# Performance work log

Measured on AMD Instinct MI355X. Metric: run time of the kernel, lower is better.

## Reference

```python
import jax, jax.numpy as jnp
import numpy as np


def setup_inputs() -> dict:
    key = jax.random.key(0)
    ks = jax.random.split(key, 6)
    B, C, H, W = 4, 64, 96, 96
    IC = C // 2
    return {
        "x": jax.random.normal(ks[0], (B, C, H, W), dtype=jnp.float32),
        "y": jax.random.normal(ks[1], (B, C, H, W), dtype=jnp.float32),
        "w_phi": jax.random.normal(ks[2], (IC, C), dtype=jnp.float32) * 0.05,
        "w_theta": jax.random.normal(ks[3], (IC, C), dtype=jnp.float32) * 0.05,
        "w_g": jax.random.normal(ks[4], (IC, C), dtype=jnp.float32) * 0.05,
        "w_mask": jax.random.normal(ks[5], (C, IC), dtype=jnp.float32) * 0.05,
    }


def reference(x, y, w_phi, w_theta, w_g, w_mask):
    # x, y: [B, C, H, W]; 1x1 convs (no bias) are channel GEMMs.
    B, C, H, W = x.shape
    IC = C // 2
    # conv outputs have IC channels, but the original views them as (B, C, -1),
    # i.e. token axis N = IC*H*W / C = H*W/2, feature axis C. Replicate exactly.
    phi = jnp.einsum('bchw,oc->bohw', x, w_phi).reshape(B, C, -1)          # [B, C, N]
    theta = jnp.einsum('bchw,oc->bohw', y, w_theta).reshape(B, C, -1)      # [B, C, N]
    theta = jnp.transpose(theta, (0, 2, 1))                                # [B, N, C]
    g = jnp.einsum('bchw,oc->bohw', x, w_g).reshape(B, C, -1)              # [B, C, N]
    g = jnp.transpose(g, (0, 2, 1))                                        # [B, N, C]
    scores = jnp.einsum('bnc,bcm->bnm', theta, phi)                        # [B, N, N]
    attn = jax.nn.softmax(scores, axis=1)  # softmax over dim=1 (rows), per original
    out = jnp.einsum('bnm,bmc->bnc', attn, g)                              # [B, N, C]
    out = jnp.transpose(out, (0, 2, 1)).reshape(B, IC, H, W)               # [B, IC, H, W]
    mask = jnp.einsum('bchw,oc->bohw', out, w_mask)                        # [B, C, H, W]
    return mask + x
```

## Files before the change

kernel.cpp:

```cpp
#include <hip/hip_runtime.h>

#define NTOK 4608
#define CCH  64
#define HWSZ 9216
#define NB   4
#define NSPL 8
#define NCHT (NTOK/32)
#define L2E  1.4426950408889634f

typedef unsigned short u16;
typedef __attribute__((ext_vector_type(4))) short s16x4;
typedef __attribute__((ext_vector_type(8))) short s16x8;
typedef __attribute__((ext_vector_type(4))) float f32x4;

__device__ __forceinline__ f32x4 mfma16(s16x8 a, s16x8 b, f32x4 c){
  return __builtin_amdgcn_mfma_f32_16x16x32_bf16(a, b, c, 0, 0, 0);
}
__device__ __forceinline__ short f2bfh(float f){
  __bf16 h = (__bf16)f;
  return (short)__builtin_bit_cast(unsigned short, h);
}
__device__ __forceinline__ float bf2f(u16 h){
  return __uint_as_float(((unsigned int)h) << 16);
}
__device__ __forceinline__ float ex2(float x){
  return __builtin_amdgcn_exp2f(x);
}

__device__ __forceinline__ void gload16(const void* g, void* l){
  __builtin_amdgcn_global_load_lds(
      (const __attribute__((address_space(1))) void*)g,
      (__attribute__((address_space(3))) void*)l, 16, 0, 0);
}
#define SBAR() __builtin_amdgcn_sched_barrier(0)
#define WAITVM(N) do{ SBAR(); asm volatile("s_waitcnt vmcnt(" #N ")" ::: "memory"); SBAR(); }while(0)
#define PRIO(N) __builtin_amdgcn_s_setprio(N)

__global__ __launch_bounds__(512) void proj_kernel(
    const float* __restrict__ x, const float* __restrict__ y,
    const float* __restrict__ w_phi, const float* __restrict__ w_theta,
    const float* __restrict__ w_g,
    u16* __restrict__ TH, u16* __restrict__ PH, u16* __restrict__ G){
  const int b = blockIdx.y;
  const int n = blockIdx.x*64 + (threadIdx.x & 63);
  const int wq = __builtin_amdgcn_readfirstlane((int)(threadIdx.x >> 6));
  const float* xb = x + (size_t)b*CCH*HWSZ;
  const float* yb = y + (size_t)b*CCH*HWSZ;
  const float* wp = w_phi   + wq*4*CCH;
  const float* wt = w_theta + wq*4*CCH;
  const float* wg = w_g     + wq*4*CCH;
  float accP[8], accT[8], accG[8];
  #pragma unroll
  for(int j=0;j<8;++j){ accP[j]=0.f; accT[j]=0.f; accG[j]=0.f; }
  for(int k=0;k<CCH;k+=4){
    float xv0[4], xv1[4], yv0[4], yv1[4];
    #pragma unroll
    for(int u=0;u<4;++u){
      xv0[u] = xb[(size_t)(k+u)*HWSZ + n];
      xv1[u] = xb[(size_t)(k+u)*HWSZ + NTOK + n];
      yv0[u] = yb[(size_t)(k+u)*HWSZ + n];
      yv1[u] = yb[(size_t)(k+u)*HWSZ + NTOK + n];
    }
    #pragma unroll
    for(int u=0;u<4;++u)
      #pragma unroll
      for(int j=0;j<8;++j){
        float xv = (j&1)?xv1[u]:xv0[u];
        accP[j] = fmaf(wp[(j>>1)*CCH + k+u], xv, accP[j]);
        accT[j] = fmaf(wt[(j>>1)*CCH + k+u], (j&1)?yv1[u]:yv0[u], accT[j]);
        accG[j] = fmaf(wg[(j>>1)*CCH + k+u], xv, accG[j]);
      }
  }
  s16x8 vp, vt;
  #pragma unroll
  for(int j=0;j<8;++j){
    vp[j]=f2bfh(accP[j]);
    vt[j]=f2bfh(accT[j]*L2E);
  }
  *(s16x8*)(PH + ((size_t)b*NTOK + n)*CCH + wq*8) = vp;
  *(s16x8*)(TH + ((size_t)b*NTOK + n)*CCH + wq*8) = vt;
  #pragma unroll
  for(int j=0;j<8;++j)
    G[((size_t)b*CCH + wq*8 + j)*NTOK + n] = f2bfh(accG[j]);
}

__global__ __launch_bounds__(256, 4) void passA_kernel(
    const u16* __restrict__ TH, const u16* __restrict__ PH,
    float* __restrict__ CSUMP){
  __shared__ __align__(16) u16 ldsTH[4*2048];
  const int bid = blockIdx.x;
  const int xcd = bid & 7, b = xcd >> 1;
  const int j = ((bid >> 3) << 1) | (xcd & 1);
  const int part = j & (NSPL-1);
  const int mt = j >> 3;
  const int lane = threadIdx.x & 63;
  const int wq = __builtin_amdgcn_readfirstlane((int)(threadIdx.x >> 6));
  const int l15 = lane & 15, lg = lane >> 4;
  const int mbase = mt*128 + wq*32;
  const u16* thb = TH + (size_t)b*NTOK*CCH;
  const u16* phb = PH + (size_t)b*NTOK*CCH;
  const u16* p0 = phb + (size_t)(mbase + l15)*CCH + lg*8;
  const u16* p1 = p0 + 16*CCH;
  s16x8 bf00 = *(const s16x8*)p0, bf01 = *(const s16x8*)(p0+32);
  s16x8 bf10 = *(const s16x8*)p1, bf11 = *(const s16x8*)(p1+32);
  float rs0 = 0.f, rs1 = 0.f;

  const int NCH = (NTOK/NSPL)/32;
  const int n0 = part*(NTOK/NSPL);
  const int srl = wq*8 + (lane>>3);
  const int ssl = (lane&7) ^ (srl&7);
  auto STAGE = [&](int ci, int bi){
    const u16* src = thb + (size_t)(n0 + ci*32 + srl)*CCH + ssl*8;
    gload16(src, ldsTH + bi*2048 + wq*512);
  };

  STAGE(0, 0); SBAR();
  STAGE(1, 1); SBAR();
  #pragma unroll 1
  for(int t=0; t<NCH; ++t){
    int ci = t+2; if(ci >= NCH) ci -= NCH;
    STAGE(ci, (t+2)&3);
    WAITVM(2);
    __builtin_amdgcn_s_barrier();
    const u16* bTH = ldsTH + (t&3)*2048;
    #pragma unroll
    for(int s=0;s<2;++s){
      const int r = s*16 + l15, rx = r & 7;
      const u16* rb = bTH + r*64;
      s16x8 a0 = *(const s16x8*)(rb + ((lg     ^ rx)<<3));
      s16x8 a1 = *(const s16x8*)(rb + (((lg+4) ^ rx)<<3));
      f32x4 v0 = {0.f,0.f,0.f,0.f}, v1 = {0.f,0.f,0.f,0.f};
      PRIO(1);
      v0 = mfma16(a0, bf00, v0); v0 = mfma16(a1, bf01, v0);
      v1 = mfma16(a0, bf10, v1); v1 = mfma16(a1, bf11, v1);
      PRIO(0);
      rs0 += (ex2(v0[0])+ex2(v0[1])) + (ex2(v0[2])+ex2(v0[3]));
      rs1 += (ex2(v1[0])+ex2(v1[1])) + (ex2(v1[2])+ex2(v1[3]));
    }
  }

  rs0 += __shfl_xor(rs0, 16); rs0 += __shfl_xor(rs0, 32);
  rs1 += __shfl_xor(rs1, 16); rs1 += __shfl_xor(rs1, 32);
  if(lg == 0){
    float* dst = CSUMP + (size_t)(part*NB + b)*NTOK + mbase;
    dst[l15]      = rs0;
    dst[16 + l15] = rs1;
  }
}

__global__ __launch_bounds__(256) void scale_g_kernel(
    const u16* __restrict__ G, const float* __restrict__ CSUMP,
    u16* __restrict__ G2){
  __shared__ float dinv[32];
  const int tid = threadIdx.x;
  const int ch = blockIdx.x % NCHT;
  const int b  = blockIdx.x / NCHT;
  const int m0 = ch*32;
  if(tid < 32){
    float s = 0.f;
    #pragma unroll
    for(int h=0;h<NSPL;++h) s += CSUMP[(size_t)(h*NB+b)*NTOK + m0 + tid];
    dinv[tid] = 1.0f/s;
  }
  __syncthreads();
  const int c  = tid & 63;
  const int lg = tid >> 6;
  const u16* gr = G + ((size_t)b*CCH + c)*NTOK + m0;
  s16x4 lo = *(const s16x4*)(gr + 4*lg);
  s16x4 hi = *(const s16x4*)(gr + 16 + 4*lg);
  s16x8 o;
  #pragma unroll
  for(int k=0;k<4;++k){
    o[k]   = f2bfh(bf2f((u16)lo[k]) * dinv[4*lg+k]);
    o[4+k] = f2bfh(bf2f((u16)hi[k]) * dinv[16+4*lg+k]);
  }
  *(s16x8*)(G2 + ((((size_t)b*NCHT + ch)*4 + lg)*CCH + c)*8) = o;
}

template<int MSPLIT>
__global__ __launch_bounds__(256, 4) void passB_kernel(
    const u16* __restrict__ TH, const u16* __restrict__ PH,
    const u16* __restrict__ G2, float* __restrict__ OUTP){
  __shared__ __align__(16) u16 ldsPH[4*2048];
  const int bid = blockIdx.x;
  const int xcd = bid & 7, b = xcd >> 1;
  const int j = ((bid >> 3) << 1) | (xcd & 1);
  const int mpart = j % MSPLIT;
  const int nt = j / MSPLIT;
  const int lane = threadIdx.x & 63;
  const int wq = __builtin_amdgcn_readfirstlane((int)(threadIdx.x >> 6));
  const int l15 = lane & 15, lg = lane >> 4;
  const int nbase = nt*128 + wq*32;
  const u16* thb = TH + (size_t)b*NTOK*CCH;
  const u16* phb = PH + (size_t)b*NTOK*CCH;
  const u16* g2b = G2 + (size_t)b*NCHT*4*CCH*8;
  const u16* t0 = thb + (size_t)(nbase + l15)*CCH + lg*8;
  const u16* t1 = t0 + 16*CCH;
  s16x8 bt00 = *(const s16x8*)t0, bt01 = *(const s16x8*)(t0+32);
  s16x8 bt10 = *(const s16x8*)t1, bt11 = *(const s16x8*)(t1+32);
  f32x4 acc[2][4];
  #pragma unroll
  for(int n2=0;n2<2;++n2)
    #pragma unroll
    for(int ct=0;ct<4;++ct) acc[n2][ct] = (f32x4){0.f,0.f,0.f,0.f};

  const int mcnt = NTOK/MSPLIT;
  const int NCH = mcnt/32;
  const int ch0 = (mpart*mcnt)/32;

  const int srl = wq*8 + (lane>>3);
  const int ssl = (lane&7) ^ (srl&7);
  auto STAGE_PH = [&](int ci, int bi){
    gload16(phb + (size_t)((ch0+ci)*32 + srl)*CCH + ssl*8,
            ldsPH + bi*2048 + wq*512);
  };

  STAGE_PH(0, 0); SBAR();
  STAGE_PH(1, 1); SBAR();
  #pragma unroll 1
  for(int t=0; t<NCH; ++t){
    WAITVM(1);
    __builtin_amdgcn_s_barrier();
    const u16* gp = g2b + ((size_t)((ch0+t)*4 + lg)*CCH + l15)*8;
    s16x8 g0 = *(const s16x8*)(gp);
    s16x8 g1 = *(const s16x8*)(gp + 128);
    s16x8 g2 = *(const s16x8*)(gp + 256);
    s16x8 g3 = *(const s16x8*)(gp + 384);
    SBAR();
    int c2 = t+2; if(c2 >= NCH) c2 -= NCH;
    STAGE_PH(c2, (t+2)&3);
    SBAR();
    const u16* bPH = ldsPH + (t&3)*2048;
    const int rx = l15 & 7;
    const u16* rb0 = bPH + l15*64;
    const u16* rb1 = rb0 + 16*64;
    s16x8 ap00 = *(const s16x8*)(rb0 + ((lg     ^ rx)<<3));
    s16x8 ap01 = *(const s16x8*)(rb0 + (((lg+4) ^ rx)<<3));
    s16x8 ap10 = *(const s16x8*)(rb1 + ((lg     ^ rx)<<3));
    s16x8 ap11 = *(const s16x8*)(rb1 + (((lg+4) ^ rx)<<3));
    f32x4 s00={0.f,0.f,0.f,0.f}, s01={0.f,0.f,0.f,0.f};
    f32x4 s10={0.f,0.f,0.f,0.f}, s11={0.f,0.f,0.f,0.f};
    PRIO(1);
    s00 = mfma16(ap00, bt00, s00); s00 = mfma16(ap01, bt01, s00);
    s01 = mfma16(ap10, bt00, s01); s01 = mfma16(ap11, bt01, s01);
    s10 = mfma16(ap00, bt10, s10); s10 = mfma16(ap01, bt11, s10);
    s11 = mfma16(ap10, bt10, s11); s11 = mfma16(ap11, bt11, s11);
    PRIO(0);
    s16x8 pa0, pa1;
    #pragma unroll
    for(int r=0;r<4;++r){
      pa0[r]   = f2bfh(ex2(s00[r]));
      pa0[4+r] = f2bfh(ex2(s01[r]));
      pa1[r]   = f2bfh(ex2(s10[r]));
      pa1[4+r] = f2bfh(ex2(s11[r]));
    }
    PRIO(1);
    acc[0][0] = mfma16(pa0, g0, acc[0][0]);
    acc[1][0] = mfma16(pa1, g0, acc[1][0]);
    acc[0][1] = mfma16(pa0, g1, acc[0][1]);
    acc[1][1] = mfma16(pa1, g1, acc[1][1]);
    acc[0][2] = mfma16(pa0, g2, acc[0][2]);
    acc[1][2] = mfma16(pa1, g2, acc[1][2]);
    acc[0][3] = mfma16(pa0, g3, acc[0][3]);
    acc[1][3] = mfma16(pa1, g3, acc[1][3]);
    PRIO(0);
  }

  float* outp = OUTP + ((size_t)(mpart*NB + b)*NTOK)*CCH;
  #pragma unroll
  for(int n2=0;n2<2;++n2)
    #pragma unroll
    for(int ct=0;ct<4;++ct)
      #pragma unroll
      for(int r=0;r<4;++r)
        outp[(size_t)(nbase + n2*16 + lg*4 + r)*CCH + ct*16 + l15] = acc[n2][ct][r];
}

__global__ __launch_bounds__(256) void reduce_kernel(
    const float* __restrict__ OUTP, float* __restrict__ OUTS, int msplit){
  const int gid = blockIdx.x*256 + threadIdx.x;
  const size_t stride4 = (size_t)NB*NTOK*CCH/4;
  const f32x4* src = (const f32x4*)OUTP;
  f32x4 a = src[gid];
  for(int h=1; h<msplit; ++h){
    f32x4 u = src[h*stride4 + gid];
    a[0]+=u[0]; a[1]+=u[1]; a[2]+=u[2]; a[3]+=u[3];
  }
  ((f32x4*)OUTS)[gid] = a;
}

__global__ __launch_bounds__(512, 2) void conv_kernel(
    const float* __restrict__ OUTS, const float* __restrict__ w_mask,
    const float* __restrict__ x, float* __restrict__ out){
  const int b = blockIdx.y;
  const int nl = threadIdx.x & 63;
  const int n = blockIdx.x*64 + nl;
  const int q = __builtin_amdgcn_readfirstlane((int)(threadIdx.x >> 6));
  const f32x4* vr = (const f32x4*)(OUTS + ((size_t)b*NTOK + n)*CCH);
  f32x4 v[16];
  #pragma unroll
  for(int k=0;k<16;++k) v[k] = vr[k];
  const float* wm = w_mask + q*8*32;
  #pragma unroll
  for(int jj=0;jj<8;++jj){
    float a0 = 0.f, a1 = 0.f;
    #pragma unroll
    for(int ic=0;ic<32;++ic){
      float w = wm[jj*32 + ic];
      a0 = fmaf(w, v[ic>>1][(2*ic)&3],   a0);
      a1 = fmaf(w, v[ic>>1][(2*ic+1)&3], a1);
    }
    const size_t idx = ((size_t)b*CCH + q*8 + jj)*HWSZ + n;
    out[idx]        = a0 + x[idx];
    out[idx + NTOK] = a1 + x[idx + NTOK];
  }
}

extern "C" void kernel_launch(void* const* d_in, const int* in_sizes, int n_in,
                              void* d_out, int out_size, void* d_ws, size_t ws_size,
                              hipStream_t stream){
  const float* x       = (const float*)d_in[0];
  const float* y       = (const float*)d_in[1];
  const float* w_phi   = (const float*)d_in[2];
  const float* w_theta = (const float*)d_in[3];
  const float* w_g     = (const float*)d_in[4];
  const float* w_mask  = (const float*)d_in[5];
  float* out = (float*)d_out;
  char* ws = (char*)d_ws;

  const size_t projB  = (size_t)NB*NTOK*CCH*sizeof(u16);
  const size_t outpB1 = (size_t)NB*NTOK*CCH*sizeof(float);
  const size_t fstat  = (size_t)NB*NTOK*sizeof(float);
  const size_t fixed  = 4*projB + (size_t)NSPL*fstat + outpB1;

  int msplit = (ws_size >= fixed + 8*outpB1) ? 8
             : (ws_size >= fixed + 4*outpB1) ? 4 : 2;

  size_t off = 0;
  u16*   TH    = (u16*)(ws + off); off += projB;
  u16*   PH    = (u16*)(ws + off); off += projB;
  u16*   G     = (u16*)(ws + off); off += projB;
  u16*   G2    = (u16*)(ws + off); off += projB;
  float* OUTP  = (float*)(ws + off); off += (size_t)msplit*outpB1;
  float* OUTS  = (float*)(ws + off); off += outpB1;
  float* CSUMP = (float*)(ws + off); off += (size_t)NSPL*fstat;

  proj_kernel<<<dim3(NTOK/64, NB), 512, 0, stream>>>(x, y, w_phi, w_theta, w_g,
                                                     TH, PH, G);
  passA_kernel<<<dim3((NTOK/128)*NSPL*NB), 256, 0, stream>>>(TH, PH, CSUMP);
  scale_g_kernel<<<dim3(NB*NCHT), 256, 0, stream>>>(G, CSUMP, G2);
  const int gB = (NTOK/128)*msplit*NB;
  switch(msplit){
    case 8: passB_kernel<8><<<dim3(gB),256,0,stream>>>(TH,PH,G2,OUTP); break;
    case 4: passB_kernel<4><<<dim3(gB),256,0,stream>>>(TH,PH,G2,OUTP); break;
    default: passB_kernel<2><<<dim3(gB),256,0,stream>>>(TH,PH,G2,OUTP); break;
  }
  reduce_kernel<<<dim3((NB*NTOK*CCH/4)/256), 256, 0, stream>>>(OUTP, OUTS, msplit);
  conv_kernel<<<dim3(NTOK/64, NB), 512, 0, stream>>>(OUTS, w_mask, x, out);
}
```

Measured before the change: 103.8 us.

## Store split-M partial outputs in bf16 and double passA staging chunk

passB now writes its per-split partial outputs as bf16 instead of fp32. The reduce and conv kernels read and write bf16 as well, which halves the intermediate traffic and the workspace they use. Separately, passA stages 64 rows of TH per pipeline step instead of 32, doing four MFMA sub-steps per barrier to amortize synchronization. Rounding partial sums to bf16 adds accuracy risk, and the larger LDS buffer may lower occupancy.

```diff
diff --git a/kernel.cpp b/kernel.cpp
--- a/kernel.cpp
+++ b/kernel.cpp
@@ -87,7 +87,7 @@
 __global__ __launch_bounds__(256, 4) void passA_kernel(
     const u16* __restrict__ TH, const u16* __restrict__ PH,
     float* __restrict__ CSUMP){
-  __shared__ __align__(16) u16 ldsTH[4*2048];
+  __shared__ __align__(16) u16 ldsTH[4*4096];
   const int bid = blockIdx.x;
   const int xcd = bid & 7, b = xcd >> 1;
   const int j = ((bid >> 3) << 1) | (xcd & 1);
@@ -105,13 +105,16 @@
   s16x8 bf10 = *(const s16x8*)p1, bf11 = *(const s16x8*)(p1+32);
   float rs0 = 0.f, rs1 = 0.f;
 
-  const int NCH = (NTOK/NSPL)/32;
+  const int NCH = (NTOK/NSPL)/64;
   const int n0 = part*(NTOK/NSPL);
-  const int srl = wq*8 + (lane>>3);
-  const int ssl = (lane&7) ^ (srl&7);
+  const int srl0 = wq*16 + (lane>>3);
+  const int ssl0 = (lane&7) ^ (srl0&7);
+  const int srl1 = srl0 + 8;
+  const int ssl1 = (lane&7) ^ (srl1&7);
   auto STAGE = [&](int ci, int bi){
-    const u16* src = thb + (size_t)(n0 + ci*32 + srl)*CCH + ssl*8;
-    gload16(src, ldsTH + bi*2048 + wq*512);
+    const u16* base = thb + (size_t)(n0 + ci*64)*CCH;
+    gload16(base + (size_t)srl0*CCH + ssl0*8, ldsTH + bi*4096 + wq*1024);
+    gload16(base + (size_t)srl1*CCH + ssl1*8, ldsTH + bi*4096 + wq*1024 + 512);
   };
 
   STAGE(0, 0); SBAR();
@@ -120,11 +123,11 @@
   for(int t=0; t<NCH; ++t){
     int ci = t+2; if(ci >= NCH) ci -= NCH;
     STAGE(ci, (t+2)&3);
-    WAITVM(2);
+    WAITVM(4);
     __builtin_amdgcn_s_barrier();
-    const u16* bTH = ldsTH + (t&3)*2048;
-    #pragma unroll
-    for(int s=0;s<2;++s){
+    const u16* bTH = ldsTH + (t&3)*4096;
+    #pragma unroll
+    for(int s=0;s<4;++s){
       const int r = s*16 + l15, rx = r & 7;
       const u16* rb = bTH + r*64;
       s16x8 a0 = *(const s16x8*)(rb + ((lg     ^ rx)<<3));
@@ -180,7 +183,7 @@
 template<int MSPLIT>
 __global__ __launch_bounds__(256, 4) void passB_kernel(
     const u16* __restrict__ TH, const u16* __restrict__ PH,
-    const u16* __restrict__ G2, float* __restrict__ OUTP){
+    const u16* __restrict__ G2, u16* __restrict__ OUTPB){
   __shared__ __align__(16) u16 ldsPH[4*2048];
   const int bid = blockIdx.x;
   const int xcd = bid & 7, b = xcd >> 1;
@@ -266,40 +269,52 @@
     PRIO(0);
   }
 
-  float* outp = OUTP + ((size_t)(mpart*NB + b)*NTOK)*CCH;
+  u16* outp = OUTPB + ((size_t)(mpart*NB + b)*NTOK)*CCH;
   #pragma unroll
   for(int n2=0;n2<2;++n2)
     #pragma unroll
     for(int ct=0;ct<4;++ct)
       #pragma unroll
       for(int r=0;r<4;++r)
-        outp[(size_t)(nbase + n2*16 + lg*4 + r)*CCH + ct*16 + l15] = acc[n2][ct][r];
+        outp[(size_t)(nbase + n2*16 + lg*4 + r)*CCH + ct*16 + l15] =
+            (u16)f2bfh(acc[n2][ct][r]);
 }
 
 __global__ __launch_bounds__(256) void reduce_kernel(
-    const float* __restrict__ OUTP, float* __restrict__ OUTS, int msplit){
+    const u16* __restrict__ OUTPB, u16* __restrict__ OUTS, int msplit){
   const int gid = blockIdx.x*256 + threadIdx.x;
-  const size_t stride4 = (size_t)NB*NTOK*CCH/4;
-  const f32x4* src = (const f32x4*)OUTP;
-  f32x4 a = src[gid];
+  const size_t stride8 = (size_t)NB*NTOK*CCH/8;
+  const s16x8* src = (const s16x8*)OUTPB;
+  float a[8];
+  s16x8 u0 = src[gid];
+  #pragma unroll
+  for(int k=0;k<8;++k) a[k] = bf2f((u16)u0[k]);
   for(int h=1; h<msplit; ++h){
-    f32x4 u = src[h*stride4 + gid];
-    a[0]+=u[0]; a[1]+=u[1]; a[2]+=u[2]; a[3]+=u[3];
-  }
-  ((f32x4*)OUTS)[gid] = a;
+    s16x8 u = src[(size_t)h*stride8 + gid];
+    #pragma unroll
+    for(int k=0;k<8;++k) a[k] += bf2f((u16)u[k]);
+  }
+  s16x8 o;
+  #pragma unroll
+  for(int k=0;k<8;++k) o[k] = f2bfh(a[k]);
+  ((s16x8*)OUTS)[gid] = o;
 }
 
 __global__ __launch_bounds__(512, 2) void conv_kernel(
-    const float* __restrict__ OUTS, const float* __restrict__ w_mask,
+    const u16* __restrict__ OUTS, const float* __restrict__ w_mask,
     const float* __restrict__ x, float* __restrict__ out){
   const int b = blockIdx.y;
   const int nl = threadIdx.x & 63;
   const int n = blockIdx.x*64 + nl;
   const int q = __builtin_amdgcn_readfirstlane((int)(threadIdx.x >> 6));
-  const f32x4* vr = (const f32x4*)(OUTS + ((size_t)b*NTOK + n)*CCH);
-  f32x4 v[16];
-  #pragma unroll
-  for(int k=0;k<16;++k) v[k] = vr[k];
+  const s16x8* vr = (const s16x8*)(OUTS + ((size_t)b*NTOK + n)*CCH);
+  float v[64];
+  #pragma unroll
+  for(int k=0;k<8;++k){
+    s16x8 u = vr[k];
+    #pragma unroll
+    for(int e=0;e<8;++e) v[k*8+e] = bf2f((u16)u[e]);
+  }
   const float* wm = w_mask + q*8*32;
   #pragma unroll
   for(int jj=0;jj<8;++jj){
@@ -307,8 +322,8 @@
     #pragma unroll
     for(int ic=0;ic<32;++ic){
       float w = wm[jj*32 + ic];
-      a0 = fmaf(w, v[ic>>1][(2*ic)&3],   a0);
-      a1 = fmaf(w, v[ic>>1][(2*ic+1)&3], a1);
+      a0 = fmaf(w, v[2*ic],   a0);
+      a1 = fmaf(w, v[2*ic+1], a1);
     }
     const size_t idx = ((size_t)b*CCH + q*8 + jj)*HWSZ + n;
     out[idx]        = a0 + x[idx];
@@ -329,20 +344,19 @@
   char* ws = (char*)d_ws;
 
   const size_t projB  = (size_t)NB*NTOK*CCH*sizeof(u16);
-  const size_t outpB1 = (size_t)NB*NTOK*CCH*sizeof(float);
   const size_t fstat  = (size_t)NB*NTOK*sizeof(float);
-  const size_t fixed  = 4*projB + (size_t)NSPL*fstat + outpB1;
-
-  int msplit = (ws_size >= fixed + 8*outpB1) ? 8
-             : (ws_size >= fixed + 4*outpB1) ? 4 : 2;
+  const size_t fixed  = 5*projB + (size_t)NSPL*fstat;
+
+  int msplit = (ws_size >= fixed + 8*projB) ? 8
+             : (ws_size >= fixed + 4*projB) ? 4 : 2;
 
   size_t off = 0;
   u16*   TH    = (u16*)(ws + off); off += projB;
   u16*   PH    = (u16*)(ws + off); off += projB;
   u16*   G     = (u16*)(ws + off); off += projB;
   u16*   G2    = (u16*)(ws + off); off += projB;
-  float* OUTP  = (float*)(ws + off); off += (size_t)msplit*outpB1;
-  float* OUTS  = (float*)(ws + off); off += outpB1;
+  u16*   OUTPB = (u16*)(ws + off); off += (size_t)msplit*projB;
+  u16*   OUTS  = (u16*)(ws + off); off += projB;
   float* CSUMP = (float*)(ws + off); off += (size_t)NSPL*fstat;
 
   proj_kernel<<<dim3(NTOK/64, NB), 512, 0, stream>>>(x, y, w_phi, w_theta, w_g,
@@ -351,10 +365,10 @@
   scale_g_kernel<<<dim3(NB*NCHT), 256, 0, stream>>>(G, CSUMP, G2);
   const int gB = (NTOK/128)*msplit*NB;
   switch(msplit){
-    case 8: passB_kernel<8><<<dim3(gB),256,0,stream>>>(TH,PH,G2,OUTP); break;
-    case 4: passB_kernel<4><<<dim3(gB),256,0,stream>>>(TH,PH,G2,OUTP); break;
-    default: passB_kernel<2><<<dim3(gB),256,0,stream>>>(TH,PH,G2,OUTP); break;
-  }
-  reduce_kernel<<<dim3((NB*NTOK*CCH/4)/256), 256, 0, stream>>>(OUTP, OUTS, msplit);
+    case 8: passB_kernel<8><<<dim3(gB),256,0,stream>>>(TH,PH,G2,OUTPB); break;
+    case 4: passB_kernel<4><<<dim3(gB),256,0,stream>>>(TH,PH,G2,OUTPB); break;
+    default: passB_kernel<2><<<dim3(gB),256,0,stream>>>(TH,PH,G2,OUTPB); break;
+  }
+  reduce_kernel<<<dim3((NB*NTOK*CCH/8)/256), 256, 0, stream>>>(OUTPB, OUTS, msplit);
   conv_kernel<<<dim3(NTOK/64, NB), 512, 0, stream>>>(OUTS, w_mask, x, out);
 }
```

After: 98.53 us. 5.1% less time.
